# Performance work log

Measured on AMD Instinct MI355X. Metric: run time of the kernel, lower is better.

## Reference

```python
import jax, jax.numpy as jnp
import numpy as np

N, T, DYN, STAT, H = 50000, 24, 16, 8, 64
E = 1_600_000


def gru_last(x, Wih, Whh, bih, bhh):
    # x: [N, T, DYN]; torch GRU gate order: r, z, n
    gx = jnp.einsum('ntd,gd->ntg', x, Wih) + bih  # [N, T, 3H]
    h0 = jnp.zeros((x.shape[0], H), x.dtype)

    def step(h, gx_t):
        gh = h @ Whh.T + bhh  # [N, 3H]
        xr, xz, xn = jnp.split(gx_t, 3, axis=-1)
        hr, hz, hn = jnp.split(gh, 3, axis=-1)
        r = jax.nn.sigmoid(xr + hr)
        z = jax.nn.sigmoid(xz + hz)
        n = jnp.tanh(xn + r * hn)
        h_new = (1.0 - z) * n + z * h
        return h_new, None

    h_last, _ = jax.lax.scan(step, h0, jnp.swapaxes(gx, 0, 1))  # scan over T
    return h_last  # [N, H]


def gcn_layer(x, W, b, src, dst, w):
    h = x @ W  # [N, out]
    msg = h[src] * w[:, None]  # gather + weight  [E, out]
    agg = jax.ops.segment_sum(msg, dst, num_segments=N)  # scatter-add
    return agg + b


def setup_inputs() -> dict:
    key = jax.random.key(0)
    ks = jax.random.split(key, 16)
    s = 0.1
    return {
        'x_dyn': jax.random.normal(ks[0], (N, T, DYN), jnp.float32),
        'x_stat': jax.random.normal(ks[1], (N, STAT), jnp.float32),
        'edge_index': jax.random.randint(ks[2], (2, E), 0, N, jnp.int32),
        'edge_weight': jax.random.uniform(ks[3], (E,), jnp.float32),
        'Wih': jax.random.normal(ks[4], (3 * H, DYN), jnp.float32) * s,
        'Whh': jax.random.normal(ks[5], (3 * H, H), jnp.float32) * s,
        'bih': jnp.zeros((3 * H,), jnp.float32),
        'bhh': jnp.zeros((3 * H,), jnp.float32),
        'W1': jax.random.normal(ks[6], (H + STAT, H), jnp.float32) * s,
        'b1': jnp.zeros((H,), jnp.float32),
        'W2': jax.random.normal(ks[7], (H, H), jnp.float32) * s,
        'b2': jnp.zeros((H,), jnp.float32),
        'Wa': jax.random.normal(ks[8], (H, 1), jnp.float32) * s,
        'ba': jnp.zeros((1,), jnp.float32),
        'Wp': jax.random.normal(ks[9], (H, 1), jnp.float32) * s,
        'bp': jnp.zeros((1,), jnp.float32),
    }


def reference(x_dyn, x_stat, edge_index, edge_weight,
              Wih, Whh, bih, bhh, W1, b1, W2, b2, Wa, ba, Wp, bp):
    src, dst = edge_index[0], edge_index[1]
    z = gru_last(x_dyn, Wih, Whh, bih, bhh)            # [N, H]
    h = jnp.concatenate([z, x_stat], axis=1)           # [N, H+STAT]
    h = jax.nn.relu(gcn_layer(h, W1, b1, src, dst, edge_weight))
    h = jax.nn.relu(gcn_layer(h, W2, b2, src, dst, edge_weight))
    # dropout omitted (eval mode)
    aqi = (h @ Wa + ba)[:, 0]
    pm = (h @ Wp + bp)[:, 0]
    return aqi, pm
```

## Files before the change

### kernel.cpp

```cpp
#include <hip/hip_runtime.h>
#include <cstdint>
#include <cstddef>

#define NNODES 50000
#define TT 24
#define DYNF 16
#define STATF 8
#define HDIM 64
#define NEDGES 1600000
#define NB 32
#define GRU_BLOCKS ((NNODES + NB - 1) / NB)
#define FILL_CHUNK 1024
#define FILL_CHUNKS ((NEDGES + FILL_CHUNK - 1) / FILL_CHUNK)
#define CAP 80
#define SLICE (NNODES / 8)
#define BINCAP 210000
#define STAGE 192
#define SCAT_BLOCKS 768

typedef __attribute__((ext_vector_type(8))) short bf16x8;
typedef __attribute__((ext_vector_type(4))) float f32x4;
typedef __attribute__((ext_vector_type(2))) float f32x2;
typedef __attribute__((ext_vector_type(2))) unsigned u32x2;

__device__ __forceinline__ unsigned short f2bf(float f) {
    unsigned u = __float_as_uint(f);
    u = (u + 0x7FFFu + ((u >> 16) & 1u)) >> 16;
    return (unsigned short)u;
}
__device__ __forceinline__ float bf2f(unsigned short s) {
    return __uint_as_float((unsigned)s << 16);
}
__device__ __forceinline__ bf16x8 cvt8(const float* __restrict__ p) {
    bf16x8 r;
    #pragma unroll
    for (int i = 0; i < 8; ++i) r[i] = (short)f2bf(p[i]);
    return r;
}
__device__ __forceinline__ bf16x8 zero8() {
    bf16x8 z;
    #pragma unroll
    for (int i = 0; i < 8; ++i) z[i] = 0;
    return z;
}
__device__ __forceinline__ float fast_tanh(float x) {
    float e = __expf(2.f * x);
    return 1.f - 2.f * __builtin_amdgcn_rcpf(e + 1.f);
}

__global__ __launch_bounds__(256) void fill_bin_kernel(
    const int* __restrict__ srcv, const int* __restrict__ dstv,
    const float* __restrict__ ew, int* __restrict__ binCnt,
    u32x2* __restrict__ bins)
{
    __shared__ u32x2 stg[8][STAGE];
    __shared__ int lcnt[8];
    __shared__ int gbase[8];
    const int tid = (int)threadIdx.x;
    const int base = (int)blockIdx.x * FILL_CHUNK;
    if (tid < 8) lcnt[tid] = 0;
    __syncthreads();
    #pragma unroll
    for (int j = 0; j < FILL_CHUNK / 256; ++j) {
        const int e = base + j * 256 + tid;
        if (e < NEDGES) {
            const int d = __builtin_nontemporal_load(dstv + e);
            const int s = __builtin_nontemporal_load(srcv + e);
            const float we = __builtin_nontemporal_load(ew + e);
            const int b = d / SLICE;
            u32x2 rec;
            rec[0] = (unsigned)s | ((unsigned)f2bf(we) << 16);
            rec[1] = (unsigned)(d - b * SLICE);
            const int pos = atomicAdd(&lcnt[b], 1);
            if (pos < STAGE) {
                stg[b][pos] = rec;
            } else {
                const int gp = atomicAdd(&binCnt[b], 1);
                if (gp < BINCAP) bins[(size_t)b * BINCAP + gp] = rec;
            }
        }
    }
    __syncthreads();
    if (tid < 8) {
        const int n = min(lcnt[tid], STAGE);
        gbase[tid] = atomicAdd(&binCnt[tid], n);
    }
    __syncthreads();
    #pragma unroll 1
    for (int b = 0; b < 8; ++b) {
        const int n = min(lcnt[b], STAGE);
        const int gb = gbase[b];
        for (int i = tid; i < n; i += 256)
            if (gb + i < BINCAP)
                bins[(size_t)b * BINCAP + gb + i] = stg[b][i];
    }
}

__global__ __launch_bounds__(256, 4) void gru_scatter_kernel(
    const float* __restrict__ x_dyn, const float* __restrict__ x_stat,
    const float* __restrict__ Wih, const float* __restrict__ Whh,
    const float* __restrict__ bih, const float* __restrict__ bhh,
    const float* __restrict__ W1, unsigned short* __restrict__ t1,
    const u32x2* __restrict__ bins, const int* __restrict__ binCnt,
    int* __restrict__ cursor, unsigned* __restrict__ csr)
{
    constexpr int S_H = 72;
    constexpr int S_X = 40;
    __shared__ short hbuf[2][NB * S_H];
    __shared__ short xbuf[2][NB * S_X];

    const int tid = (int)threadIdx.x;

    if ((int)blockIdx.x >= GRU_BLOCKS) {
        const int fb = (int)blockIdx.x - GRU_BLOCKS;
        const int slice = fb & 7;
        const int sub   = fb >> 3;
        const int lo    = slice * SLICE;
        const int cnt   = min(binCnt[slice], BINCAP);
        const u32x2* __restrict__ mybin = bins + (size_t)slice * BINCAP;
        for (int i = sub * 256 + tid; i < cnt; i += (SCAT_BLOCKS / 8) * 256) {
            const u32x2 r = __builtin_nontemporal_load(mybin + i);
            const int d = lo + (int)r[1];
            const int pos = atomicAdd(&cursor[d], 1);
            if (pos < CAP) csr[(size_t)d * CAP + pos] = r[0];
        }
        return;
    }

    const int lane = tid & 63;
    const int w = __builtin_amdgcn_readfirstlane(tid >> 6);
    const int col = lane & 15;
    const int quad = lane >> 4;
    const int node0 = (int)blockIdx.x * NB;

    bf16x8 Bh[3][2];
    bf16x8 Bx[3];
    #pragma unroll
    for (int g = 0; g < 3; ++g) {
        const int n = (w + g * 4) * 16 + col;
        #pragma unroll
        for (int kt = 0; kt < 2; ++kt)
            Bh[g][kt] = cvt8(Whh + (size_t)n * HDIM + kt * 32 + quad * 8);
        Bx[g] = (quad < 2) ? cvt8(Wih + (size_t)n * DYNF + quad * 8) : zero8();
    }

    const int jg = w * 16 + col;
    const float b_r  = bih[jg]        + bhh[jg];
    const float b_z  = bih[HDIM + jg] + bhh[HDIM + jg];
    const float b_xn = bih[2 * HDIM + jg];
    const float b_hn = bhh[2 * HDIM + jg];

    for (int i = tid; i < NB * S_H; i += 256) hbuf[0][i] = 0;

    auto stage_x = [&](int t, int b) {
        const int nd = tid >> 3, c = tid & 7;
        int node = node0 + nd;
        if (node >= NNODES) node = 0;
        const f32x2 v = __builtin_nontemporal_load(
            reinterpret_cast<const f32x2*>(
                x_dyn + (size_t)node * (TT * DYNF) + t * DYNF + c * 2));
        unsigned pk = (unsigned)f2bf(v[0]) | ((unsigned)f2bf(v[1]) << 16);
        *reinterpret_cast<unsigned*>(&xbuf[b][nd * S_X + c * 2]) = pk;
        *reinterpret_cast<unsigned*>(&xbuf[b][nd * S_X + 16 + c * 2]) = 0u;
    };
    stage_x(0, 0);

    float hprev[2][4];
    #pragma unroll
    for (int mt = 0; mt < 2; ++mt)
        #pragma unroll
        for (int r = 0; r < 4; ++r) hprev[mt][r] = 0.f;

    for (int t = 0; t < TT; ++t) {
        const int rb = t & 1;
        __syncthreads();

        f32x4 accr[2], accz[2], accnh[2], accnx[2];
        #pragma unroll
        for (int mt = 0; mt < 2; ++mt) {
            const int nd = mt * 16 + col;
            const bf16x8 a0 = *reinterpret_cast<const bf16x8*>(&hbuf[rb][nd * S_H + quad * 8]);
            const bf16x8 a1 = *reinterpret_cast<const bf16x8*>(&hbuf[rb][nd * S_H + 32 + quad * 8]);
            const bf16x8 ax = *reinterpret_cast<const bf16x8*>(&xbuf[rb][nd * S_X + quad * 8]);
            const f32x4 z4 = {0.f, 0.f, 0.f, 0.f};
            accr[mt]  = __builtin_amdgcn_mfma_f32_16x16x32_bf16(a0, Bh[0][0], z4, 0, 0, 0);
            accr[mt]  = __builtin_amdgcn_mfma_f32_16x16x32_bf16(a1, Bh[0][1], accr[mt], 0, 0, 0);
            accr[mt]  = __builtin_amdgcn_mfma_f32_16x16x32_bf16(ax, Bx[0],    accr[mt], 0, 0, 0);
            accz[mt]  = __builtin_amdgcn_mfma_f32_16x16x32_bf16(a0, Bh[1][0], z4, 0, 0, 0);
            accz[mt]  = __builtin_amdgcn_mfma_f32_16x16x32_bf16(a1, Bh[1][1], accz[mt], 0, 0, 0);
            accz[mt]  = __builtin_amdgcn_mfma_f32_16x16x32_bf16(ax, Bx[1],    accz[mt], 0, 0, 0);
            accnh[mt] = __builtin_amdgcn_mfma_f32_16x16x32_bf16(a0, Bh[2][0], z4, 0, 0, 0);
            accnh[mt] = __builtin_amdgcn_mfma_f32_16x16x32_bf16(a1, Bh[2][1], accnh[mt], 0, 0, 0);
            accnx[mt] = __builtin_amdgcn_mfma_f32_16x16x32_bf16(ax, Bx[2],    z4, 0, 0, 0);
        }

        if (t + 1 < TT) stage_x(t + 1, rb ^ 1);

        #pragma unroll
        for (int mt = 0; mt < 2; ++mt) {
            #pragma unroll
            for (int r = 0; r < 4; ++r) {
                const float dr = 1.f + __expf(-(accr[mt][r] + b_r));
                const float dz = 1.f + __expf(-(accz[mt][r] + b_z));
                const float q  = __builtin_amdgcn_rcpf(dr * dz);
                const float R  = q * dz;
                const float Z  = q * dr;
                const float Nn = fast_tanh(accnx[mt][r] + b_xn + R * (accnh[mt][r] + b_hn));
                const float hn = Nn + Z * (hprev[mt][r] - Nn);
                hprev[mt][r] = hn;
                hbuf[rb ^ 1][(mt * 16 + quad * 4 + r) * S_H + jg] = (short)f2bf(hn);
            }
        }
    }
    __syncthreads();

    bf16x8 Bw0, Bw1, Bw2;
    #pragma unroll
    for (int j = 0; j < 8; ++j) {
        Bw0[j] = (short)f2bf(W1[(size_t)(quad * 8 + j) * HDIM + jg]);
        Bw1[j] = (short)f2bf(W1[(size_t)(32 + quad * 8 + j) * HDIM + jg]);
    }
    if (quad == 0) {
        #pragma unroll
        for (int j = 0; j < 8; ++j)
            Bw2[j] = (short)f2bf(W1[(size_t)(HDIM + j) * HDIM + jg]);
    } else {
        Bw2 = zero8();
    }

    #pragma unroll
    for (int mt = 0; mt < 2; ++mt) {
        const int nd = mt * 16 + col;
        const bf16x8 a0 = *reinterpret_cast<const bf16x8*>(&hbuf[0][nd * S_H + quad * 8]);
        const bf16x8 a1 = *reinterpret_cast<const bf16x8*>(&hbuf[0][nd * S_H + 32 + quad * 8]);
        bf16x8 axs;
        if (quad == 0) {
            int node = node0 + nd;
            if (node >= NNODES) node = 0;
            axs = cvt8(x_stat + (size_t)node * STATF);
        } else {
            axs = zero8();
        }
        const f32x4 z4 = {0.f, 0.f, 0.f, 0.f};
        f32x4 aw;
        aw = __builtin_amdgcn_mfma_f32_16x16x32_bf16(a0, Bw0, z4, 0, 0, 0);
        aw = __builtin_amdgcn_mfma_f32_16x16x32_bf16(a1, Bw1, aw, 0, 0, 0);
        aw = __builtin_amdgcn_mfma_f32_16x16x32_bf16(axs, Bw2, aw, 0, 0, 0);
        #pragma unroll
        for (int r = 0; r < 4; ++r) {
            const int node = node0 + mt * 16 + quad * 4 + r;
            if (node < NNODES) t1[(size_t)node * HDIM + jg] = f2bf(aw[r]);
        }
    }
}

__global__ __launch_bounds__(256) void gather_transform_kernel(
    const unsigned short* __restrict__ tsrc, const int* __restrict__ cursor,
    const unsigned* __restrict__ csr, const float* __restrict__ b1,
    const float* __restrict__ W2, unsigned short* __restrict__ out)
{
    __shared__ float aggL[16][68];
    const int tid  = (int)threadIdx.x;
    const int lane = tid & 63;
    const int w    = tid >> 6;
    const int q    = lane >> 4;
    const int f    = lane & 15;
    const int node0 = (int)blockIdx.x * 16;
    const int jg = w * 16 + f;

    bf16x8 Bw0, Bw1;
    float bk0[8], bk1[8];
    #pragma unroll
    for (int j = 0; j < 8; ++j) {
        Bw0[j] = (short)f2bf(W2[(size_t)(q * 8 + j) * HDIM + jg]);
        Bw1[j] = (short)f2bf(W2[(size_t)(32 + q * 8 + j) * HDIM + jg]);
        bk0[j] = b1[q * 8 + j];
        bk1[j] = b1[32 + q * 8 + j];
    }

    int pn[4], en[4], bg[4];
    float a[4][4];
    #pragma unroll
    for (int n = 0; n < 4; ++n) {
        const int node = node0 + w * 4 + n;
        bg[n] = node * CAP;
        const int cnt = min(cursor[node], CAP);
        pn[n] = bg[n] + q;
        en[n] = bg[n] + cnt;
        #pragma unroll
        for (int j = 0; j < 4; ++j) a[n][j] = 0.f;
    }

    bool more = (pn[0] < en[0]) | (pn[1] < en[1]) |
                (pn[2] < en[2]) | (pn[3] < en[3]);
    while (__any(more)) {
        bool act[4];
        unsigned e[4];
        #pragma unroll
        for (int n = 0; n < 4; ++n) {
            act[n] = pn[n] < en[n];
            e[n] = csr[act[n] ? pn[n] : bg[n]];
        }
        u32x2 r[4];
        #pragma unroll
        for (int n = 0; n < 4; ++n) {
            const int src = act[n] ? (int)(e[n] & 0xFFFFu) : 0;
            r[n] = *reinterpret_cast<const u32x2*>(
                tsrc + (size_t)src * HDIM + 4 * f);
        }
        #pragma unroll
        for (int n = 0; n < 4; ++n) {
            const float wg = act[n] ? __uint_as_float(e[n] & 0xFFFF0000u) : 0.f;
            a[n][0] += wg * bf2f((unsigned short)(r[n][0] & 0xFFFFu));
            a[n][1] += wg * bf2f((unsigned short)(r[n][0] >> 16));
            a[n][2] += wg * bf2f((unsigned short)(r[n][1] & 0xFFFFu));
            a[n][3] += wg * bf2f((unsigned short)(r[n][1] >> 16));
            pn[n] += 4;
        }
        more = (pn[0] < en[0]) | (pn[1] < en[1]) |
               (pn[2] < en[2]) | (pn[3] < en[3]);
    }

    #pragma unroll
    for (int n = 0; n < 4; ++n)
        #pragma unroll
        for (int j = 0; j < 4; ++j) {
            a[n][j] += __shfl_xor(a[n][j], 16, 64);
            a[n][j] += __shfl_xor(a[n][j], 32, 64);
        }
    if (lane < 16) {
        #pragma unroll
        for (int n = 0; n < 4; ++n) {
            f32x4 o; o[0] = a[n][0]; o[1] = a[n][1]; o[2] = a[n][2]; o[3] = a[n][3];
            *reinterpret_cast<f32x4*>(&aggL[w * 4 + n][4 * f]) = o;
        }
    }
    __syncthreads();

    bf16x8 fa0, fa1;
    #pragma unroll
    for (int j = 0; j < 8; ++j) {
        fa0[j] = (short)f2bf(fmaxf(aggL[f][q * 8 + j] + bk0[j], 0.f));
        fa1[j] = (short)f2bf(fmaxf(aggL[f][32 + q * 8 + j] + bk1[j], 0.f));
    }
    const f32x4 z4 = {0.f, 0.f, 0.f, 0.f};
    f32x4 aw;
    aw = __builtin_amdgcn_mfma_f32_16x16x32_bf16(fa0, Bw0, z4, 0, 0, 0);
    aw = __builtin_amdgcn_mfma_f32_16x16x32_bf16(fa1, Bw1, aw, 0, 0, 0);
    #pragma unroll
    for (int r = 0; r < 4; ++r)
        out[(size_t)(node0 + q * 4 + r) * HDIM + jg] = f2bf(aw[r]);
}

__global__ __launch_bounds__(256) void gather_head_kernel(
    const unsigned short* __restrict__ tsrc, const int* __restrict__ cursor,
    const unsigned* __restrict__ csr,
    const float* __restrict__ b2, const float* __restrict__ Wa,
    const float* __restrict__ ba, const float* __restrict__ Wp,
    const float* __restrict__ bp, float* __restrict__ out)
{
    const int tid  = (int)threadIdx.x;
    const int lane = tid & 63;
    const int w    = tid >> 6;
    const int q    = lane >> 4;
    const int f    = lane & 15;
    const int node0 = (int)blockIdx.x * 16;

    int pn[4], en[4], bg[4];
    float a[4][4];
    #pragma unroll
    for (int n = 0; n < 4; ++n) {
        const int node = node0 + w * 4 + n;
        bg[n] = node * CAP;
        const int cnt = min(cursor[node], CAP);
        pn[n] = bg[n] + q;
        en[n] = bg[n] + cnt;
        #pragma unroll
        for (int j = 0; j < 4; ++j) a[n][j] = 0.f;
    }

    bool more = (pn[0] < en[0]) | (pn[1] < en[1]) |
                (pn[2] < en[2]) | (pn[3] < en[3]);
    while (__any(more)) {
        bool act[4];
        unsigned e[4];
        #pragma unroll
        for (int n = 0; n < 4; ++n) {
            act[n] = pn[n] < en[n];
            e[n] = csr[act[n] ? pn[n] : bg[n]];
        }
        u32x2 r[4];
        #pragma unroll
        for (int n = 0; n < 4; ++n) {
            const int src = act[n] ? (int)(e[n] & 0xFFFFu) : 0;
            r[n] = *reinterpret_cast<const u32x2*>(
                tsrc + (size_t)src * HDIM + 4 * f);
        }
        #pragma unroll
        for (int n = 0; n < 4; ++n) {
            const float wg = act[n] ? __uint_as_float(e[n] & 0xFFFF0000u) : 0.f;
            a[n][0] += wg * bf2f((unsigned short)(r[n][0] & 0xFFFFu));
            a[n][1] += wg * bf2f((unsigned short)(r[n][0] >> 16));
            a[n][2] += wg * bf2f((unsigned short)(r[n][1] & 0xFFFFu));
            a[n][3] += wg * bf2f((unsigned short)(r[n][1] >> 16));
            pn[n] += 4;
        }
        more = (pn[0] < en[0]) | (pn[1] < en[1]) |
               (pn[2] < en[2]) | (pn[3] < en[3]);
    }

    #pragma unroll
    for (int n = 0; n < 4; ++n)
        #pragma unroll
        for (int j = 0; j < 4; ++j) {
            a[n][j] += __shfl_xor(a[n][j], 16, 64);
            a[n][j] += __shfl_xor(a[n][j], 32, 64);
        }

    const f32x4 bb = *reinterpret_cast<const f32x4*>(b2 + 4 * f);
    const f32x4 wa = *reinterpret_cast<const f32x4*>(Wa + 4 * f);
    const f32x4 wp = *reinterpret_cast<const f32x4*>(Wp + 4 * f);
    float sa[4], sp[4];
    #pragma unroll
    for (int n = 0; n < 4; ++n) {
        const float h0 = fmaxf(a[n][0] + bb[0], 0.f);
        const float h1 = fmaxf(a[n][1] + bb[1], 0.f);
        const float h2 = fmaxf(a[n][2] + bb[2], 0.f);
        const float h3 = fmaxf(a[n][3] + bb[3], 0.f);
        sa[n] = h0 * wa[0] + h1 * wa[1] + h2 * wa[2] + h3 * wa[3];
        sp[n] = h0 * wp[0] + h1 * wp[1] + h2 * wp[2] + h3 * wp[3];
        #pragma unroll
        for (int off = 1; off < 16; off <<= 1) {
            sa[n] += __shfl_xor(sa[n], off, 64);
            sp[n] += __shfl_xor(sp[n], off, 64);
        }
    }
    if (lane == 0) {
        #pragma unroll
        for (int n = 0; n < 4; ++n) {
            const int node = node0 + w * 4 + n;
            out[node] = sa[n] + ba[0];
            out[NNODES + node] = sp[n] + bp[0];
        }
    }
}

extern "C" void kernel_launch(void* const* d_in, const int* in_sizes, int n_in,
                              void* d_out, int out_size, void* d_ws, size_t ws_size,
                              hipStream_t stream)
{
    const float* x_dyn  = (const float*)d_in[0];
    const float* x_stat = (const float*)d_in[1];
    const int*   eidx   = (const int*)  d_in[2];
    const float* ew     = (const float*)d_in[3];
    const float* Wih    = (const float*)d_in[4];
    const float* Whh    = (const float*)d_in[5];
    const float* bih    = (const float*)d_in[6];
    const float* bhh    = (const float*)d_in[7];
    const float* W1     = (const float*)d_in[8];
    const float* b1     = (const float*)d_in[9];
    const float* W2     = (const float*)d_in[10];
    const float* b2     = (const float*)d_in[11];
    const float* Wa     = (const float*)d_in[12];
    const float* ba     = (const float*)d_in[13];
    const float* Wp     = (const float*)d_in[14];
    const float* bp     = (const float*)d_in[15];

    const int* srcv = eidx;
    const int* dstv = eidx + NEDGES;

    unsigned short* t1 = (unsigned short*)d_ws;
    unsigned short* t2 = t1 + (size_t)NNODES * HDIM;
    unsigned* csr = (unsigned*)(t2 + (size_t)NNODES * HDIM);
    int* cursor = (int*)(csr + (size_t)NNODES * CAP);
    int* binCnt = cursor + NNODES;
    u32x2* bins = (u32x2*)(binCnt + 16);

    dim3 blk(256);

    hipMemsetAsync(cursor, 0, (size_t)(NNODES + 16) * sizeof(int), stream);

    fill_bin_kernel<<<dim3(FILL_CHUNKS), blk, 0, stream>>>(
        srcv, dstv, ew, binCnt, bins);

    gru_scatter_kernel<<<dim3(GRU_BLOCKS + SCAT_BLOCKS), blk, 0, stream>>>(
        x_dyn, x_stat, Wih, Whh, bih, bhh, W1, t1,
        bins, binCnt, cursor, csr);

    gather_transform_kernel<<<dim3(NNODES / 16), blk, 0, stream>>>(
        t1, cursor, csr, b1, W2, t2);

    gather_head_kernel<<<dim3(NNODES / 16), blk, 0, stream>>>(
        t2, cursor, csr, b2, Wa, ba, Wp, bp, (float*)d_out);
}
```

Baseline: 343.5 us.

## Split CSR gathers into two source-range sweeps and reorder scatter blocks first

Both gather kernels now walk each node's edge list twice, and each pass only gathers sources from one half of the node range. This keeps the hot part of the bf16 feature table smaller so it fits better in cache. CSR entries are read with nontemporal loads. The fused GRU/scatter kernel now assigns its low block indices to the scatter work, so those blocks are dispatched before the GRU blocks. The cost is reading every CSR entry twice and extra loop overhead, including wasted dummy loads for inactive lanes.

After: 469.8 us. 36.8% more time.

```diff
diff --git a/kernel.cpp b/kernel.cpp
--- a/kernel.cpp
+++ b/kernel.cpp
@@ -17,6 +17,7 @@
 #define BINCAP 210000
 #define STAGE 192
 #define SCAT_BLOCKS 768
+#define HALF (NNODES / 2)
 
 typedef __attribute__((ext_vector_type(8))) short bf16x8;
 typedef __attribute__((ext_vector_type(4))) float f32x4;
@@ -111,8 +112,8 @@
 
     const int tid = (int)threadIdx.x;
 
-    if ((int)blockIdx.x >= GRU_BLOCKS) {
-        const int fb = (int)blockIdx.x - GRU_BLOCKS;
+    if ((int)blockIdx.x < SCAT_BLOCKS) {
+        const int fb = (int)blockIdx.x;
         const int slice = fb & 7;
         const int sub   = fb >> 3;
         const int lo    = slice * SLICE;
@@ -131,7 +132,7 @@
     const int w = __builtin_amdgcn_readfirstlane(tid >> 6);
     const int col = lane & 15;
     const int quad = lane >> 4;
-    const int node0 = (int)blockIdx.x * NB;
+    const int node0 = ((int)blockIdx.x - SCAT_BLOCKS) * NB;
 
     bf16x8 Bh[3][2];
     bf16x8 Bx[3];
@@ -278,47 +279,53 @@
         bk1[j] = b1[32 + q * 8 + j];
     }
 
-    int pn[4], en[4], bg[4];
+    int en[4], bg[4];
     float a[4][4];
     #pragma unroll
     for (int n = 0; n < 4; ++n) {
         const int node = node0 + w * 4 + n;
         bg[n] = node * CAP;
-        const int cnt = min(cursor[node], CAP);
-        pn[n] = bg[n] + q;
-        en[n] = bg[n] + cnt;
+        en[n] = bg[n] + min(cursor[node], CAP);
         #pragma unroll
         for (int j = 0; j < 4; ++j) a[n][j] = 0.f;
     }
 
-    bool more = (pn[0] < en[0]) | (pn[1] < en[1]) |
-                (pn[2] < en[2]) | (pn[3] < en[3]);
-    while (__any(more)) {
-        bool act[4];
-        unsigned e[4];
-        #pragma unroll
-        for (int n = 0; n < 4; ++n) {
-            act[n] = pn[n] < en[n];
-            e[n] = csr[act[n] ? pn[n] : bg[n]];
-        }
-        u32x2 r[4];
-        #pragma unroll
-        for (int n = 0; n < 4; ++n) {
-            const int src = act[n] ? (int)(e[n] & 0xFFFFu) : 0;
-            r[n] = *reinterpret_cast<const u32x2*>(
-                tsrc + (size_t)src * HDIM + 4 * f);
-        }
-        #pragma unroll
-        for (int n = 0; n < 4; ++n) {
-            const float wg = act[n] ? __uint_as_float(e[n] & 0xFFFF0000u) : 0.f;
-            a[n][0] += wg * bf2f((unsigned short)(r[n][0] & 0xFFFFu));
-            a[n][1] += wg * bf2f((unsigned short)(r[n][0] >> 16));
-            a[n][2] += wg * bf2f((unsigned short)(r[n][1] & 0xFFFFu));
-            a[n][3] += wg * bf2f((unsigned short)(r[n][1] >> 16));
-            pn[n] += 4;
-        }
-        more = (pn[0] < en[0]) | (pn[1] < en[1]) |
-               (pn[2] < en[2]) | (pn[3] < en[3]);
+    #pragma unroll 1
+    for (int sweep = 0; sweep < 2; ++sweep) {
+        const unsigned slo = (unsigned)(sweep * HALF);
+        int pn[4];
+        #pragma unroll
+        for (int n = 0; n < 4; ++n) pn[n] = bg[n] + q;
+        bool more = (pn[0] < en[0]) | (pn[1] < en[1]) |
+                    (pn[2] < en[2]) | (pn[3] < en[3]);
+        while (__any(more)) {
+            bool use[4];
+            unsigned e[4];
+            #pragma unroll
+            for (int n = 0; n < 4; ++n) {
+                const bool act = pn[n] < en[n];
+                e[n] = __builtin_nontemporal_load(&csr[act ? pn[n] : bg[n]]);
+                use[n] = act && ((e[n] & 0xFFFFu) - slo < (unsigned)HALF);
+            }
+            u32x2 r[4];
+            #pragma unroll
+            for (int n = 0; n < 4; ++n) {
+                const unsigned src = use[n] ? (e[n] & 0xFFFFu) : slo;
+                r[n] = *reinterpret_cast<const u32x2*>(
+                    tsrc + (size_t)src * HDIM + 4 * f);
+            }
+            #pragma unroll
+            for (int n = 0; n < 4; ++n) {
+                const float wg = use[n] ? __uint_as_float(e[n] & 0xFFFF0000u) : 0.f;
+                a[n][0] += wg * bf2f((unsigned short)(r[n][0] & 0xFFFFu));
+                a[n][1] += wg * bf2f((unsigned short)(r[n][0] >> 16));
+                a[n][2] += wg * bf2f((unsigned short)(r[n][1] & 0xFFFFu));
+                a[n][3] += wg * bf2f((unsigned short)(r[n][1] >> 16));
+                pn[n] += 4;
+            }
+            more = (pn[0] < en[0]) | (pn[1] < en[1]) |
+                   (pn[2] < en[2]) | (pn[3] < en[3]);
+        }
     }
 
     #pragma unroll
@@ -366,47 +373,53 @@
     const int f    = lane & 15;
     const int node0 = (int)blockIdx.x * 16;
 
-    int pn[4], en[4], bg[4];
+    int en[4], bg[4];
     float a[4][4];
     #pragma unroll
     for (int n = 0; n < 4; ++n) {
         const int node = node0 + w * 4 + n;
         bg[n] = node * CAP;
-        const int cnt = min(cursor[node], CAP);
-        pn[n] = bg[n] + q;
-        en[n] = bg[n] + cnt;
+        en[n] = bg[n] + min(cursor[node], CAP);
         #pragma unroll
         for (int j = 0; j < 4; ++j) a[n][j] = 0.f;
     }
 
-    bool more = (pn[0] < en[0]) | (pn[1] < en[1]) |
-                (pn[2] < en[2]) | (pn[3] < en[3]);
-    while (__any(more)) {
-        bool act[4];
-        unsigned e[4];
-        #pragma unroll
-        for (int n = 0; n < 4; ++n) {
-            act[n] = pn[n] < en[n];
-            e[n] = csr[act[n] ? pn[n] : bg[n]];
-        }
-        u32x2 r[4];
-        #pragma unroll
-        for (int n = 0; n < 4; ++n) {
-            const int src = act[n] ? (int)(e[n] & 0xFFFFu) : 0;
-            r[n] = *reinterpret_cast<const u32x2*>(
-                tsrc + (size_t)src * HDIM + 4 * f);
-        }
-        #pragma unroll
-        for (int n = 0; n < 4; ++n) {
-            const float wg = act[n] ? __uint_as_float(e[n] & 0xFFFF0000u) : 0.f;
-            a[n][0] += wg * bf2f((unsigned short)(r[n][0] & 0xFFFFu));
-            a[n][1] += wg * bf2f((unsigned short)(r[n][0] >> 16));
-            a[n][2] += wg * bf2f((unsigned short)(r[n][1] & 0xFFFFu));
-            a[n][3] += wg * bf2f((unsigned short)(r[n][1] >> 16));
-            pn[n] += 4;
-        }
-        more = (pn[0] < en[0]) | (pn[1] < en[1]) |
-               (pn[2] < en[2]) | (pn[3] < en[3]);
+    #pragma unroll 1
+    for (int sweep = 0; sweep < 2; ++sweep) {
+        const unsigned slo = (unsigned)(sweep * HALF);
+        int pn[4];
+        #pragma unroll
+        for (int n = 0; n < 4; ++n) pn[n] = bg[n] + q;
+        bool more = (pn[0] < en[0]) | (pn[1] < en[1]) |
+                    (pn[2] < en[2]) | (pn[3] < en[3]);
+        while (__any(more)) {
+            bool use[4];
+            unsigned e[4];
+            #pragma unroll
+            for (int n = 0; n < 4; ++n) {
+                const bool act = pn[n] < en[n];
+                e[n] = __builtin_nontemporal_load(&csr[act ? pn[n] : bg[n]]);
+                use[n] = act && ((e[n] & 0xFFFFu) - slo < (unsigned)HALF);
+            }
+            u32x2 r[4];
+            #pragma unroll
+            for (int n = 0; n < 4; ++n) {
+                const unsigned src = use[n] ? (e[n] & 0xFFFFu) : slo;
+                r[n] = *reinterpret_cast<const u32x2*>(
+                    tsrc + (size_t)src * HDIM + 4 * f);
+            }
+            #pragma unroll
+            for (int n = 0; n < 4; ++n) {
+                const float wg = use[n] ? __uint_as_float(e[n] & 0xFFFF0000u) : 0.f;
+                a[n][0] += wg * bf2f((unsigned short)(r[n][0] & 0xFFFFu));
+                a[n][1] += wg * bf2f((unsigned short)(r[n][0] >> 16));
+                a[n][2] += wg * bf2f((unsigned short)(r[n][1] & 0xFFFFu));
+                a[n][3] += wg * bf2f((unsigned short)(r[n][1] >> 16));
+                pn[n] += 4;
+            }
+            more = (pn[0] < en[0]) | (pn[1] < en[1]) |
+                   (pn[2] < en[2]) | (pn[3] < en[3]);
+        }
     }
 
     #pragma unroll
```
